# Kernel tuning notes

Measured on AMD Instinct MI355X. Metric: run time of the kernel, lower is better.

## Reference

```python
import jax, jax.numpy as jnp
import numpy as np

B, S, CIN = 16384, 24, 10
NH, DK, DM = 16, 8, 256
DV = DM // NH  # 16
EPS = 1e-5
T_POS = 1000.0


def _ln(x, g, b):
    mu = jnp.mean(x, axis=-1, keepdims=True)
    var = jnp.mean((x - mu) ** 2, axis=-1, keepdims=True)
    return (x - mu) * jax.lax.rsqrt(var + EPS) * g + b


def _bn(x, g, b, m, v):
    # eval-mode BatchNorm1d over channel (last) dim
    return (x - m) * jax.lax.rsqrt(v + EPS) * g + b


def setup_inputs() -> dict:
    key = jax.random.key(0)
    ks = jax.random.split(key, 16)
    x = jax.random.normal(ks[0], (B, S, CIN + 1), dtype=jnp.float32)
    pos = jax.random.uniform(ks[1], (B, S), dtype=jnp.float32) * 365.0
    x = x.at[:, :, 0].set(pos)
    w = lambda k, shp, s=0.05: (jax.random.normal(k, shp, dtype=jnp.float32) * s)
    d = {
        'x': x,
        'ln1_g': jnp.ones((CIN,), jnp.float32), 'ln1_b': jnp.zeros((CIN,), jnp.float32),
        'conv_w': w(ks[2], (DM, CIN)), 'conv_b': jnp.zeros((DM,), jnp.float32),
        'bn1_g': jnp.ones((DM,), jnp.float32), 'bn1_b': jnp.zeros((DM,), jnp.float32),
        'bn1_m': jnp.zeros((DM,), jnp.float32), 'bn1_v': jnp.ones((DM,), jnp.float32),
        'Q': w(ks[3], (NH, DK), float(np.sqrt(2.0 / DK))),
        'Wk': w(ks[4], (NH * DK, DM), float(np.sqrt(2.0 / DK))), 'bk': jnp.zeros((NH * DK,), jnp.float32),
        'W1': w(ks[5], (128, 256)), 'b1': jnp.zeros((128,), jnp.float32),
        'bn2_g': jnp.ones((128,), jnp.float32), 'bn2_b': jnp.zeros((128,), jnp.float32),
        'bn2_m': jnp.zeros((128,), jnp.float32), 'bn2_v': jnp.ones((128,), jnp.float32),
        'oln_g': jnp.ones((128,), jnp.float32), 'oln_b': jnp.zeros((128,), jnp.float32),
        'Wd1': w(ks[6], (64, 128)), 'bd1': jnp.zeros((64,), jnp.float32),
        'bnd1_g': jnp.ones((64,), jnp.float32), 'bnd1_b': jnp.zeros((64,), jnp.float32),
        'bnd1_m': jnp.zeros((64,), jnp.float32), 'bnd1_v': jnp.ones((64,), jnp.float32),
        'Wd2': w(ks[7], (32, 64)), 'bd2': jnp.zeros((32,), jnp.float32),
        'bnd2_g': jnp.ones((32,), jnp.float32), 'bnd2_b': jnp.zeros((32,), jnp.float32),
        'bnd2_m': jnp.zeros((32,), jnp.float32), 'bnd2_v': jnp.ones((32,), jnp.float32),
        'Wd3': w(ks[8], (20, 32)), 'bd3': jnp.zeros((20,), jnp.float32),
    }
    return d


def reference(x, ln1_g, ln1_b, conv_w, conv_b, bn1_g, bn1_b, bn1_m, bn1_v,
              Q, Wk, bk, W1, b1, bn2_g, bn2_b, bn2_m, bn2_v, oln_g, oln_b,
              Wd1, bd1, bnd1_g, bnd1_b, bnd1_m, bnd1_v,
              Wd2, bd2, bnd2_g, bnd2_b, bnd2_m, bnd2_v, Wd3, bd3):
    pos = x[:, :, 0]            # (B, S) positions
    feat = x[:, :, 1:]          # (B, S, CIN)
    feat = _ln(feat, ln1_g, ln1_b)
    # inconv: 1x1 Conv1d == per-timestep Linear, then eval BatchNorm1d over channels
    h = jnp.einsum('bsc,dc->bsd', feat, conv_w) + conv_b
    h = _bn(h, bn1_g, bn1_b, bn1_m, bn1_v)
    # sinusoid positional encoding, interleaved sin/cos
    div = jnp.exp(jnp.arange(0, DM, 2, dtype=jnp.float32) * (-np.log(T_POS) / DM))  # (DM/2,)
    ang = pos[:, :, None] * div                                   # (B, S, DM/2)
    pe = jnp.stack([jnp.sin(ang), jnp.cos(ang)], axis=-1).reshape(pos.shape[0], pos.shape[1], DM)
    e = h + pe                                                    # (B, S, DM)
    # LTAE multi-head attention with shared learned query
    k = jnp.einsum('bsd,hkd->bshk', e, Wk.reshape(NH, DK, DM)) + bk.reshape(NH, DK)
    logits = jnp.einsum('hk,bshk->bhs', Q, k) / np.sqrt(DK)
    attn = jax.nn.softmax(logits, axis=-1)                        # (B, NH, S); dropout=eval
    v = e.reshape(e.shape[0], e.shape[1], NH, DV)                 # head-chunked values
    o = jnp.einsum('bhs,bshc->bhc', attn, v).reshape(e.shape[0], NH * DV)  # (B, 256)
    # MLP3: Linear(256,128) + BN + ReLU, then dropout(eval) + LayerNorm
    m = jax.nn.relu(_bn(o @ W1.T + b1, bn2_g, bn2_b, bn2_m, bn2_v))
    m = _ln(m, oln_g, oln_b)
    # decoder: [128,64,32,20]
    d1 = jax.nn.relu(_bn(m @ Wd1.T + bd1, bnd1_g, bnd1_b, bnd1_m, bnd1_v))
    d2 = jax.nn.relu(_bn(d1 @ Wd2.T + bd2, bnd2_g, bnd2_b, bnd2_m, bnd2_v))
    out = d2 @ Wd3.T + bd3                                        # (B, 20)
    return out
```

## Files before the change

### kernel.cpp

```cpp
#include <hip/hip_runtime.h>
#include <hip/hip_bf16.h>


typedef __attribute__((ext_vector_type(8))) short bf16x8;
typedef __attribute__((ext_vector_type(4))) float f32x4;

#define EPS 1e-5f
#define INV_SQRT8 0.35355339059327373f
#define KDIV (-0.07785768972392256f)
#define INV2PI 0.15915494309189535f
#define LOG2E 1.4426950408889634f

__device__ __forceinline__ unsigned short f2bf(float f){
  union { float f; unsigned u; } v; v.f = f;
  unsigned r = v.u + 0x7FFFu + ((v.u >> 16) & 1u);
  return (unsigned short)(r >> 16);
}
__device__ __forceinline__ float bf2f(unsigned short h){
  union { unsigned u; float f; } v; v.u = ((unsigned)h) << 16; return v.f;
}
__device__ __forceinline__ float asf(unsigned u){
  union { unsigned u; float f; } v; v.u = u; return v.f;
}
__device__ __forceinline__ unsigned pk2bf(float lo, float hi){
  __hip_bfloat162 h2 = __float22bfloat162_rn(make_float2(lo, hi));
  return *reinterpret_cast<unsigned*>(&h2);
}

__global__ __launch_bounds__(256) void k0_pre(
    const float* __restrict__ conv_w, const float* __restrict__ conv_b,
    const float* __restrict__ bn1_g, const float* __restrict__ bn1_b,
    const float* __restrict__ bn1_m, const float* __restrict__ bn1_v,
    const float* __restrict__ Q, const float* __restrict__ Wk,
    const float* __restrict__ bk,
    const float* __restrict__ W1, const float* __restrict__ b1,
    const float* __restrict__ bn2_g, const float* __restrict__ bn2_b,
    const float* __restrict__ bn2_m, const float* __restrict__ bn2_v,
    const float* __restrict__ oln_g, const float* __restrict__ oln_b,
    const float* __restrict__ Wd1, const float* __restrict__ bd1,
    const float* __restrict__ bnd1_g, const float* __restrict__ bnd1_b,
    const float* __restrict__ bnd1_m, const float* __restrict__ bnd1_v,
    const float* __restrict__ Wd2, const float* __restrict__ bd2,
    const float* __restrict__ bnd2_g, const float* __restrict__ bnd2_b,
    const float* __restrict__ bnd2_m, const float* __restrict__ bnd2_v,
    const float* __restrict__ Wd3,
    unsigned short* __restrict__ wqF, unsigned short* __restrict__ w1F,
    unsigned short* __restrict__ wd1F, unsigned short* __restrict__ wd2F,
    unsigned short* __restrict__ wd3F,
    float* __restrict__ convwT, float* __restrict__ convbE,
    float* __restrict__ biasq, float* __restrict__ b1E,
    float* __restrict__ bd1E, float* __restrict__ bd2E)
{
  __shared__ float redL[256];
  const int t = threadIdx.x;
  const int bid = blockIdx.x;

  if (bid < 64){
    for (int e = bid*512 + t; e < bid*512 + 512; e += 256){
      int j = e & 7, lj = (e >> 3) & 63, kc = (e >> 9) & 7, nt = (e >> 12) & 7;
      int n = nt*16 + (lj & 15);
      int k = kc*32 + ((lj >> 4) << 3) + j;
      float s2 = bn2_g[n] * rsqrtf(bn2_v[n] + EPS);
      w1F[e] = f2bf(W1[n*256 + k] * s2);
    }
  } else if (bid < 68){
    int base = (bid - 64)*2048;
    #pragma unroll 4
    for (int it = 0; it < 8; ++it){
      int e = base + it*256 + t;
      int j = e & 7, lj = (e >> 3) & 63, kc = (e >> 9) & 3, nt = (e >> 11) & 3;
      int n = nt*16 + (lj & 15);
      int k = kc*32 + ((lj >> 4) << 3) + j;
      float sd = bnd1_g[n] * rsqrtf(bnd1_v[n] + EPS);
      wd1F[e] = f2bf(Wd1[n*128 + k] * sd * oln_g[k]);
    }
  } else if (bid == 68){
    #pragma unroll 4
    for (int it = 0; it < 8; ++it){
      int e = it*256 + t;
      int j = e & 7, lj = (e >> 3) & 63, kc = (e >> 9) & 1, nt = (e >> 10) & 1;
      int n = nt*16 + (lj & 15);
      int k = kc*32 + ((lj >> 4) << 3) + j;
      float sd = bnd2_g[n] * rsqrtf(bnd2_v[n] + EPS);
      wd2F[e] = f2bf(Wd2[n*64 + k] * sd);
    }
  } else if (bid == 69){
    #pragma unroll
    for (int it = 0; it < 4; ++it){
      int e = it*256 + t;
      int j = e & 7, lj = (e >> 3) & 63, nt = (e >> 9) & 1;
      int n = nt*16 + (lj & 15);
      int k = ((lj >> 4) << 3) + j;
      float v = (n < 20) ? Wd3[n*32 + k] : 0.f;
      wd3F[e] = f2bf(v);
    }
  } else if (bid == 70){
    #pragma unroll 4
    for (int it = 0; it < 16; ++it){
      int e = it*256 + t;
      int j = e & 7, lj = (e >> 3) & 63, kc = (e >> 9) & 7;
      int h = lj & 15;
      int dd = kc*32 + ((lj >> 4) << 3) + j;
      float acc = 0.f;
      #pragma unroll
      for (int kk = 0; kk < 8; ++kk)
        acc += Q[h*8+kk] * Wk[(h*8+kk)*256 + dd];
      wqF[e] = f2bf(acc * INV_SQRT8);
    }
  } else if (bid == 71){
    __shared__ float wqL[16*257];
    __shared__ float coefL[256*12];
    __shared__ float QL[128];
    __shared__ float bkL[128];
    wqF[4096 + t] = 0; wqF[4096 + 256 + t] = 0;
    if (t < 128){ QL[t] = Q[t]; bkL[t] = bk[t]; }
    __syncthreads();
    {
      const int d = t;
      float s1 = bn1_g[d] * rsqrtf(bn1_v[d] + EPS);
      #pragma unroll
      for (int c = 0; c < 10; ++c) coefL[d*12 + c] = conv_w[d*10 + c] * s1;
      coefL[d*12 + 10] = conv_b[d]*s1 + bn1_b[d] - bn1_m[d]*s1;
      coefL[d*12 + 11] = 0.f;
      #pragma unroll 4
      for (int h = 0; h < 16; ++h){
        float acc = 0.f;
        #pragma unroll
        for (int kk = 0; kk < 8; ++kk)
          acc += QL[h*8+kk] * Wk[(h*8+kk)*256 + d];
        wqL[h*257 + d] = acc;
      }
    }
    __syncthreads();
    if (t < 176){
      int h = t / 11, cc = t - h*11;
      const float* wq = wqL + h*257;
      float acc = 0.f;
      #pragma unroll 4
      for (int d2 = 0; d2 < 256; ++d2)
        acc += coefL[d2*12 + cc] * wq[d2];
      acc *= INV_SQRT8;
      if (cc < 10){
        int lane = (cc < 8) ? h : (16 + h);
        int j = cc & 7;
        wqF[4096 + lane*8 + j] = f2bf(acc);
      } else {
        float qb = 0.f;
        #pragma unroll
        for (int kk = 0; kk < 8; ++kk) qb += QL[h*8+kk]*bkL[h*8+kk];
        biasq[h] = acc + qb * INV_SQRT8;
      }
    }
  } else if (bid == 72){
    #pragma unroll
    for (int it = 0; it < 10; ++it){
      int e = it*256 + t;
      int c = e >> 8, d = e & 255;
      float s1 = bn1_g[d] * rsqrtf(bn1_v[d] + EPS);
      convwT[e] = conv_w[d*10 + c] * s1;
    }
  } else if (bid == 73){
    {
      int d = t;
      float s1 = bn1_g[d] * rsqrtf(bn1_v[d] + EPS);
      convbE[d] = conv_b[d]*s1 + bn1_b[d] - bn1_m[d]*s1;
    }
    if (t < 128){
      float s2 = bn2_g[t] * rsqrtf(bn2_v[t] + EPS);
      b1E[t] = b1[t]*s2 + bn2_b[t] - bn2_m[t]*s2;
    }
    if (t < 32){
      float sd = bnd2_g[t] * rsqrtf(bnd2_v[t] + EPS);
      bd2E[t] = bd2[t]*sd + bnd2_b[t] - bnd2_m[t]*sd;
    }
  } else {
    int n = t >> 2, si = t & 3;
    float acc = 0.f;
    #pragma unroll 8
    for (int i2 = 0; i2 < 32; ++i2){
      int i = si*32 + i2;
      acc += oln_b[i] * Wd1[n*128 + i];
    }
    redL[t] = acc;
    __syncthreads();
    if (t < 64){
      float sd = bnd1_g[t] * rsqrtf(bnd1_v[t] + EPS);
      float a = redL[4*t] + redL[4*t+1] + redL[4*t+2] + redL[4*t+3];
      bd1E[t] = bd1[t]*sd + bnd1_b[t] - bnd1_m[t]*sd + a*sd;
    }
  }
}

__global__ __launch_bounds__(256, 4) void k1_attn(
    const float* __restrict__ x, const float* __restrict__ ln1_g,
    const float* __restrict__ ln1_b,
    const unsigned short* __restrict__ wqF, const float* __restrict__ convwT,
    const float* __restrict__ convbE, const float* __restrict__ biasq,
    unsigned short* __restrict__ o_frag)
{
  __shared__ unsigned short peR[48*264];
  __shared__ float attnF[2*16*25];
  __shared__ unsigned short featn[48*16];
  __shared__ float xL[528];
  __shared__ float divL[128];
  __shared__ __align__(16) unsigned short zeroB[8];
  float* gL = xL;

  const int t = threadIdx.x;
  const int b0 = blockIdx.x * 2;
  const int w = t >> 6, l = t & 63;

  if (t < 132)
    *(float4*)(xL + t*4) = *(const float4*)(x + (size_t)b0*264 + t*4);
  if (t < 128) divL[t] = exp2f((float)t * KDIV) * INV2PI;
  if (t < 8) zeroB[t] = 0;
  __syncthreads();

  if (w == 3){
    if (l < 48){
      const float* xr = xL + l*11;
      float f[10]; float mu = 0.f;
      #pragma unroll
      for (int c = 0; c < 10; ++c){ f[c] = xr[1+c]; mu += f[c]; }
      mu *= 0.1f;
      float var = 0.f;
      #pragma unroll
      for (int c = 0; c < 10; ++c){ float dv = f[c]-mu; var += dv*dv; }
      var *= 0.1f;
      float rs = rsqrtf(var + EPS);
      float fn[10];
      #pragma unroll
      for (int c = 0; c < 10; ++c) fn[c] = (f[c]-mu)*rs*ln1_g[c] + ln1_b[c];
      #pragma unroll
      for (int q = 0; q < 5; ++q)
        *(unsigned*)(featn + l*16 + 2*q) = pk2bf(fn[2*q], fn[2*q+1]);
      #pragma unroll
      for (int z = 0; z < 3; ++z)
        *(unsigned*)(featn + l*16 + 10 + 2*z) = 0u;
    }
  }

  f32x4 acc = {0.f,0.f,0.f,0.f};
  const int m = l & 15, g = l >> 4;
  if (w < 3){
    const int mt = w;
    const int row = mt*16 + m;
    const float p = xL[row*11];
    #pragma unroll
    for (int kc = 0; kc < 8; ++kc){
      float4 dv4 = *(const float4*)(divL + kc*16 + g*4);
      unsigned pk[4];
      #pragma unroll
      for (int q = 0; q < 4; ++q){
        float dv = (q==0)?dv4.x:(q==1)?dv4.y:(q==2)?dv4.z:dv4.w;
        float ang = p * dv;
        float fr = ang - floorf(ang);
        float sv = __builtin_amdgcn_sinf(fr);
        float cv = __builtin_amdgcn_cosf(fr);
        pk[q] = pk2bf(sv, cv);
      }
      union { bf16x8 v; uint4 u; } af;
      af.u = make_uint4(pk[0], pk[1], pk[2], pk[3]);
      *(uint4*)(peR + row*264 + (kc*4+g)*8) = af.u;
      bf16x8 b = *(const bf16x8*)(wqF + ((size_t)(kc*64 + l))*8);
      acc = __builtin_amdgcn_mfma_f32_16x16x32_bf16(af.v, b, acc, 0, 0, 0);
    }
  }
  __syncthreads();

  if (w < 3){
    const int mt = w;
    {
      const unsigned short* ap = (g < 2) ? (featn + (mt*16 + m)*16 + g*8)
                                         : zeroB;
      bf16x8 a = *(const bf16x8*)ap;
      bf16x8 b = *(const bf16x8*)(wqF + ((size_t)(8*64 + l))*8);
      acc = __builtin_amdgcn_mfma_f32_16x16x32_bf16(a, b, acc, 0, 0, 0);
    }
    const int h = m;
    float bq = biasq[h];
    #pragma unroll
    for (int reg = 0; reg < 4; ++reg){
      int row = mt*16 + g*4 + reg;
      int bb = row >= 24; int s = row - bb*24;
      attnF[(bb*16+h)*25 + s] = acc[reg] + bq;
    }
  }
  __syncthreads();

  {
    const int bh = t >> 3, ln = t & 7;
    float* L = attnF + bh*25;
    float v0 = L[ln], v1 = L[ln+8], v2 = L[ln+16];
    float mx = fmaxf(fmaxf(v0, v1), v2);
    mx = fmaxf(mx, __shfl_xor(mx, 1, 64));
    mx = fmaxf(mx, __shfl_xor(mx, 2, 64));
    mx = fmaxf(mx, __shfl_xor(mx, 4, 64));
    float p0 = exp2f((v0-mx)*LOG2E);
    float p1 = exp2f((v1-mx)*LOG2E);
    float p2 = exp2f((v2-mx)*LOG2E);
    float sm = p0 + p1 + p2;
    sm += __shfl_xor(sm, 1, 64);
    sm += __shfl_xor(sm, 2, 64);
    sm += __shfl_xor(sm, 4, 64);
    float inv = 1.f / sm;
    L[ln] = p0*inv; L[ln+8] = p1*inv; L[ln+16] = p2*inv;
  }
  __syncthreads();

  if (t < 160){
    int bb = t / 80; int rem = t - bb*80;
    int h = rem / 5, c = rem - h*5;
    const float* A = attnF + (bb*16+h)*25;
    float g0 = 0.f, g1 = 0.f;
    for (int s = 0; s < 24; ++s){
      float a = A[s];
      const unsigned short* fr = featn + (bb*24+s)*16;
      g0 += a * bf2f(fr[c]);
      g1 += a * bf2f(fr[c+5]);
    }
    gL[(bb*16+h)*12 + c]     = g0;
    gL[(bb*16+h)*12 + c + 5] = g1;
  }
  __syncthreads();

  {
    const int bb = t >> 7, dp = t & 127;
    const int d0 = dp*2, h = dp >> 3;
    float2 o2 = *(const float2*)(convbE + d0);
    const float* gp = gL + (bb*16+h)*12;
    #pragma unroll
    for (int c = 0; c < 10; ++c){
      float2 cw = *(const float2*)(convwT + c*256 + d0);
      o2.x += cw.x * gp[c];
      o2.y += cw.y * gp[c];
    }
    const float* A = attnF + (bb*16+h)*25;
    const unsigned short* pr = peR + bb*24*264 + d0;
    #pragma unroll
    for (int s = 0; s < 24; ++s){
      unsigned u = *(const unsigned*)(pr + s*264);
      float a = A[s];
      o2.x += a * asf(u << 16);
      o2.y += a * asf(u & 0xFFFF0000u);
    }
    const int row = b0 + bb;
    const int rt = row >> 4, mm = row & 15;
    const int kc = d0 >> 5, gg = (d0 >> 3) & 3, j = d0 & 7;
    *(unsigned*)(o_frag + ((size_t)((rt*8+kc)*64 + gg*16 + mm))*8 + j)
        = pk2bf(o2.x, o2.y);
  }
}

__global__ __launch_bounds__(256, 4) void k2_mlp(
    const unsigned short* __restrict__ o_frag,
    const unsigned short* __restrict__ w1F, const float* __restrict__ b1E,
    const unsigned short* __restrict__ wd1F, const float* __restrict__ bd1E,
    const unsigned short* __restrict__ wd2F, const float* __restrict__ bd2E,
    const unsigned short* __restrict__ wd3F, const float* __restrict__ bd3,
    float* __restrict__ out)
{
  __shared__ float mL[16*132];
  __shared__ unsigned short mh[16*136];
  __shared__ unsigned short d1L[16*72];
  __shared__ unsigned short d2L[16*40];
  __shared__ float redL[64];
  __shared__ float stats[32];

  const int t = threadIdx.x;
  const int w = t >> 6, l = t & 63;
  const size_t rowBase = (size_t)blockIdx.x * 16;
  const int rt = blockIdx.x;
  const int g8  = (l >> 4) << 3;
  const int c15 = l & 15;

  {
    f32x4 acc[2];
    { f32x4 z = {0.f,0.f,0.f,0.f}; acc[0] = z; acc[1] = z; }
    #pragma unroll
    for (int kc = 0; kc < 8; ++kc){
      bf16x8 a = *(const bf16x8*)(o_frag + ((size_t)((rt*8+kc)*64 + l))*8);
      #pragma unroll
      for (int n2 = 0; n2 < 2; ++n2){
        int nt = 2*w + n2;
        bf16x8 b = *(const bf16x8*)(w1F + ((size_t)((nt*8+kc)*64 + l))*8);
        acc[n2] = __builtin_amdgcn_mfma_f32_16x16x32_bf16(a, b, acc[n2], 0,0,0);
      }
    }
    #pragma unroll
    for (int n2 = 0; n2 < 2; ++n2){
      int col = (2*w + n2)*16 + c15;
      float be = b1E[col];
      #pragma unroll
      for (int reg = 0; reg < 4; ++reg){
        int row = ((l>>4)<<2) + reg;
        mL[row*132 + col] = fmaxf(acc[n2][reg] + be, 0.f);
      }
    }
  }
  __syncthreads();

  if (t < 32){
    const float* R = mL + (t>>1)*132 + (t&1)*64;
    float s = 0.f, q = 0.f;
    for (int k = 0; k < 64; ++k){ float v = R[k]; s += v; q += v*v; }
    redL[t*2] = s; redL[t*2+1] = q;
  }
  __syncthreads();
  if (t < 16){
    float s = redL[4*t] + redL[4*t+2];
    float q = redL[4*t+1] + redL[4*t+3];
    float mu = s * (1.f/128.f);
    float var = q * (1.f/128.f) - mu*mu;
    stats[2*t] = mu; stats[2*t+1] = rsqrtf(var + EPS);
  }
  __syncthreads();

  {
    int r = t >> 4, run = t & 15;
    float mu = stats[2*r], rs = stats[2*r+1];
    const float* R = mL + r*132 + run*8;
    unsigned pk[4];
    #pragma unroll
    for (int q = 0; q < 4; ++q)
      pk[q] = pk2bf((R[2*q]-mu)*rs, (R[2*q+1]-mu)*rs);
    *(uint4*)(mh + r*136 + run*8) = make_uint4(pk[0], pk[1], pk[2], pk[3]);
  }
  __syncthreads();

  {
    const int nt = w;
    f32x4 acc = {0.f,0.f,0.f,0.f};
    #pragma unroll
    for (int kc = 0; kc < 4; ++kc){
      bf16x8 b = *(const bf16x8*)(wd1F + ((size_t)((nt*4+kc)*64 + l))*8);
      bf16x8 a = *(const bf16x8*)(mh + c15*136 + kc*32 + g8);
      acc = __builtin_amdgcn_mfma_f32_16x16x32_bf16(a, b, acc, 0,0,0);
    }
    int col = nt*16 + c15;
    float be = bd1E[col];
    #pragma unroll
    for (int reg = 0; reg < 4; ++reg){
      int row = ((l>>4)<<2) + reg;
      d1L[row*72 + col] = f2bf(fmaxf(acc[reg] + be, 0.f));
    }
  }
  __syncthreads();

  if (w < 2){
    const int nt = w;
    f32x4 acc = {0.f,0.f,0.f,0.f};
    #pragma unroll
    for (int kc = 0; kc < 2; ++kc){
      bf16x8 a = *(const bf16x8*)(d1L + c15*72 + kc*32 + g8);
      bf16x8 b = *(const bf16x8*)(wd2F + ((size_t)((nt*2+kc)*64 + l))*8);
      acc = __builtin_amdgcn_mfma_f32_16x16x32_bf16(a, b, acc, 0,0,0);
    }
    int col = nt*16 + c15;
    float be = bd2E[col];
    #pragma unroll
    for (int reg = 0; reg < 4; ++reg){
      int row = ((l>>4)<<2) + reg;
      d2L[row*40 + col] = f2bf(fmaxf(acc[reg] + be, 0.f));
    }
  }
  __syncthreads();

  if (w < 2){
    const int nt = w;
    bf16x8 a = *(const bf16x8*)(d2L + c15*40 + g8);
    bf16x8 b = *(const bf16x8*)(wd3F + ((size_t)(nt*64 + l))*8);
    f32x4 acc = {0.f,0.f,0.f,0.f};
    acc = __builtin_amdgcn_mfma_f32_16x16x32_bf16(a, b, acc, 0,0,0);
    int col = nt*16 + c15;
    if (col < 20){
      float be = bd3[col];
      #pragma unroll
      for (int reg = 0; reg < 4; ++reg){
        int row = ((l>>4)<<2) + reg;
        out[(rowBase + row)*20 + col] = acc[reg] + be;
      }
    }
  }
}

extern "C" void kernel_launch(void* const* d_in, const int* in_sizes, int n_in,
                              void* d_out, int out_size, void* d_ws, size_t ws_size,
                              hipStream_t stream)
{
  (void)in_sizes; (void)n_in; (void)out_size; (void)ws_size;
  const float* x      = (const float*)d_in[0];
  const float* ln1_g  = (const float*)d_in[1];
  const float* ln1_b  = (const float*)d_in[2];
  const float* conv_w = (const float*)d_in[3];
  const float* conv_b = (const float*)d_in[4];
  const float* bn1_g  = (const float*)d_in[5];
  const float* bn1_b  = (const float*)d_in[6];
  const float* bn1_m  = (const float*)d_in[7];
  const float* bn1_v  = (const float*)d_in[8];
  const float* Q      = (const float*)d_in[9];
  const float* Wk     = (const float*)d_in[10];
  const float* bk     = (const float*)d_in[11];
  const float* W1     = (const float*)d_in[12];
  const float* b1     = (const float*)d_in[13];
  const float* bn2_g  = (const float*)d_in[14];
  const float* bn2_b  = (const float*)d_in[15];
  const float* bn2_m  = (const float*)d_in[16];
  const float* bn2_v  = (const float*)d_in[17];
  const float* oln_g  = (const float*)d_in[18];
  const float* oln_b  = (const float*)d_in[19];
  const float* Wd1    = (const float*)d_in[20];
  const float* bd1    = (const float*)d_in[21];
  const float* bnd1_g = (const float*)d_in[22];
  const float* bnd1_b = (const float*)d_in[23];
  const float* bnd1_m = (const float*)d_in[24];
  const float* bnd1_v = (const float*)d_in[25];
  const float* Wd2    = (const float*)d_in[26];
  const float* bd2    = (const float*)d_in[27];
  const float* bnd2_g = (const float*)d_in[28];
  const float* bnd2_b = (const float*)d_in[29];
  const float* bnd2_m = (const float*)d_in[30];
  const float* bnd2_v = (const float*)d_in[31];
  const float* Wd3    = (const float*)d_in[32];
  const float* bd3    = (const float*)d_in[33];

  char* ws = (char*)d_ws;
  unsigned short* wqF  = (unsigned short*)(ws + 0);
  unsigned short* w1F  = (unsigned short*)(ws + 9216);
  unsigned short* wd1F = (unsigned short*)(ws + 74752);
  unsigned short* wd2F = (unsigned short*)(ws + 91136);
  unsigned short* wd3F = (unsigned short*)(ws + 95232);
  float* convwT = (float*)(ws + 97280);
  float* convbE = (float*)(ws + 107520);
  float* biasq  = (float*)(ws + 108544);
  float* b1E    = (float*)(ws + 108608);
  float* bd1E   = (float*)(ws + 109120);
  float* bd2E   = (float*)(ws + 109376);
  unsigned short* o_frag = (unsigned short*)(ws + 109568);

  hipLaunchKernelGGL(k0_pre, dim3(75), dim3(256), 0, stream,
      conv_w, conv_b, bn1_g, bn1_b, bn1_m, bn1_v, Q, Wk, bk,
      W1, b1, bn2_g, bn2_b, bn2_m, bn2_v, oln_g, oln_b,
      Wd1, bd1, bnd1_g, bnd1_b, bnd1_m, bnd1_v,
      Wd2, bd2, bnd2_g, bnd2_b, bnd2_m, bnd2_v, Wd3,
      wqF, w1F, wd1F, wd2F, wd3F, convwT, convbE, biasq, b1E, bd1E, bd2E);

  hipLaunchKernelGGL(k1_attn, dim3(8192), dim3(256), 0, stream,
      x, ln1_g, ln1_b, wqF, convwT, convbE, biasq, o_frag);

  hipLaunchKernelGGL(k2_mlp, dim3(1024), dim3(256), 0, stream,
      o_frag, w1F, b1E, wd1F, bd1E, wd2F, bd2E, wd3F, bd3, (float*)d_out);
}
```

Baseline: 186.0 us.

## Spread positional-encoding generation over all warps and use MFMA for attention-weighted features

Positional-encoding sin/cos generation now runs across all four warps instead of three, and the attention-logit MFMA reads the encoding back from shared memory after a barrier. The attention-weighted feature reduction is recast as a 16x16x32 bf16 MFMA per batch element, replacing a scalar loop over 160 threads. Attention rows are also packed at stride 24 so they can be read with float4 loads into registers. The intent is better warp balance and fewer scalar LDS reads, at the cost of an extra shared-memory round trip and bf16 rounding of the attention weights in the feature path.

```diff
diff --git a/kernel.cpp b/kernel.cpp
--- a/kernel.cpp
+++ b/kernel.cpp
@@ -198,12 +198,11 @@
     const float* __restrict__ convbE, const float* __restrict__ biasq,
     unsigned short* __restrict__ o_frag)
 {
-  __shared__ unsigned short peR[48*264];
-  __shared__ float attnF[2*16*25];
-  __shared__ unsigned short featn[48*16];
-  __shared__ float xL[528];
-  __shared__ float divL[128];
-  __shared__ __align__(16) unsigned short zeroB[8];
+  __shared__ __align__(16) unsigned short peR[48*264];
+  __shared__ __align__(16) float attnF[32*24];
+  __shared__ __align__(16) unsigned short featn[48*16];
+  __shared__ __align__(16) float divL[128];
+  __shared__ __align__(16) float xL[536];
   float* gL = xL;
 
   const int t = threadIdx.x;
@@ -212,85 +211,82 @@
 
   if (t < 132)
     *(float4*)(xL + t*4) = *(const float4*)(x + (size_t)b0*264 + t*4);
+  else if (t < 134)
+    *(float4*)(xL + 528 + (t-132)*4) = make_float4(0.f,0.f,0.f,0.f);
   if (t < 128) divL[t] = exp2f((float)t * KDIV) * INV2PI;
-  if (t < 8) zeroB[t] = 0;
-  __syncthreads();
-
-  if (w == 3){
-    if (l < 48){
-      const float* xr = xL + l*11;
-      float f[10]; float mu = 0.f;
-      #pragma unroll
-      for (int c = 0; c < 10; ++c){ f[c] = xr[1+c]; mu += f[c]; }
-      mu *= 0.1f;
-      float var = 0.f;
-      #pragma unroll
-      for (int c = 0; c < 10; ++c){ float dv = f[c]-mu; var += dv*dv; }
-      var *= 0.1f;
-      float rs = rsqrtf(var + EPS);
-      float fn[10];
-      #pragma unroll
-      for (int c = 0; c < 10; ++c) fn[c] = (f[c]-mu)*rs*ln1_g[c] + ln1_b[c];
-      #pragma unroll
-      for (int q = 0; q < 5; ++q)
-        *(unsigned*)(featn + l*16 + 2*q) = pk2bf(fn[2*q], fn[2*q+1]);
-      #pragma unroll
-      for (int z = 0; z < 3; ++z)
-        *(unsigned*)(featn + l*16 + 10 + 2*z) = 0u;
-    }
-  }
-
-  f32x4 acc = {0.f,0.f,0.f,0.f};
+  __syncthreads();
+
+  {
+    const int g = (l >> 4) & 3, rlo = l & 15;
+    #pragma unroll
+    for (int it = 0; it < 6; ++it){
+      int combo = it*4 + w;
+      int mt = combo >> 3, kc = combo & 7;
+      int row = mt*16 + rlo;
+      int run = kc*4 + g;
+      float p = xL[row*11];
+      unsigned pk[4];
+      #pragma unroll
+      for (int q = 0; q < 4; ++q){
+        float fr = __builtin_amdgcn_fractf(p * divL[run*4 + q]);
+        pk[q] = pk2bf(__builtin_amdgcn_sinf(fr), __builtin_amdgcn_cosf(fr));
+      }
+      *(uint4*)(peR + row*264 + run*8) = make_uint4(pk[0], pk[1], pk[2], pk[3]);
+    }
+  }
+  if (w == 3 && l < 48){
+    const float* xr = xL + l*11;
+    float f[10]; float mu = 0.f;
+    #pragma unroll
+    for (int c = 0; c < 10; ++c){ f[c] = xr[1+c]; mu += f[c]; }
+    mu *= 0.1f;
+    float var = 0.f;
+    #pragma unroll
+    for (int c = 0; c < 10; ++c){ float dv = f[c]-mu; var += dv*dv; }
+    var *= 0.1f;
+    float rs = rsqrtf(var + EPS);
+    float fn[10];
+    #pragma unroll
+    for (int c = 0; c < 10; ++c) fn[c] = (f[c]-mu)*rs*ln1_g[c] + ln1_b[c];
+    #pragma unroll
+    for (int q = 0; q < 5; ++q)
+      *(unsigned*)(featn + l*16 + 2*q) = pk2bf(fn[2*q], fn[2*q+1]);
+    #pragma unroll
+    for (int z = 0; z < 3; ++z)
+      *(unsigned*)(featn + l*16 + 10 + 2*z) = 0u;
+  }
+  __syncthreads();
+
   const int m = l & 15, g = l >> 4;
   if (w < 3){
     const int mt = w;
-    const int row = mt*16 + m;
-    const float p = xL[row*11];
+    f32x4 acc = {0.f,0.f,0.f,0.f};
     #pragma unroll
     for (int kc = 0; kc < 8; ++kc){
-      float4 dv4 = *(const float4*)(divL + kc*16 + g*4);
-      unsigned pk[4];
-      #pragma unroll
-      for (int q = 0; q < 4; ++q){
-        float dv = (q==0)?dv4.x:(q==1)?dv4.y:(q==2)?dv4.z:dv4.w;
-        float ang = p * dv;
-        float fr = ang - floorf(ang);
-        float sv = __builtin_amdgcn_sinf(fr);
-        float cv = __builtin_amdgcn_cosf(fr);
-        pk[q] = pk2bf(sv, cv);
-      }
-      union { bf16x8 v; uint4 u; } af;
-      af.u = make_uint4(pk[0], pk[1], pk[2], pk[3]);
-      *(uint4*)(peR + row*264 + (kc*4+g)*8) = af.u;
+      bf16x8 a = *(const bf16x8*)(peR + (mt*16 + m)*264 + kc*32 + g*8);
       bf16x8 b = *(const bf16x8*)(wqF + ((size_t)(kc*64 + l))*8);
-      acc = __builtin_amdgcn_mfma_f32_16x16x32_bf16(af.v, b, acc, 0, 0, 0);
-    }
-  }
-  __syncthreads();
-
-  if (w < 3){
-    const int mt = w;
+      acc = __builtin_amdgcn_mfma_f32_16x16x32_bf16(a, b, acc, 0, 0, 0);
+    }
     {
       const unsigned short* ap = (g < 2) ? (featn + (mt*16 + m)*16 + g*8)
-                                         : zeroB;
+                                         : (const unsigned short*)(xL + 528);
       bf16x8 a = *(const bf16x8*)ap;
       bf16x8 b = *(const bf16x8*)(wqF + ((size_t)(8*64 + l))*8);
       acc = __builtin_amdgcn_mfma_f32_16x16x32_bf16(a, b, acc, 0, 0, 0);
     }
-    const int h = m;
-    float bq = biasq[h];
+    float bq = biasq[m];
     #pragma unroll
     for (int reg = 0; reg < 4; ++reg){
       int row = mt*16 + g*4 + reg;
       int bb = row >= 24; int s = row - bb*24;
-      attnF[(bb*16+h)*25 + s] = acc[reg] + bq;
+      attnF[(bb*16+m)*24 + s] = acc[reg] + bq;
     }
   }
   __syncthreads();
 
   {
     const int bh = t >> 3, ln = t & 7;
-    float* L = attnF + bh*25;
+    float* L = attnF + bh*24;
     float v0 = L[ln], v1 = L[ln+8], v2 = L[ln+16];
     float mx = fmaxf(fmaxf(v0, v1), v2);
     mx = fmaxf(mx, __shfl_xor(mx, 1, 64));
@@ -308,19 +304,34 @@
   }
   __syncthreads();
 
-  if (t < 160){
-    int bb = t / 80; int rem = t - bb*80;
-    int h = rem / 5, c = rem - h*5;
-    const float* A = attnF + (bb*16+h)*25;
-    float g0 = 0.f, g1 = 0.f;
-    for (int s = 0; s < 24; ++s){
-      float a = A[s];
-      const unsigned short* fr = featn + (bb*24+s)*16;
-      g0 += a * bf2f(fr[c]);
-      g1 += a * bf2f(fr[c+5]);
-    }
-    gL[(bb*16+h)*12 + c]     = g0;
-    gL[(bb*16+h)*12 + c + 5] = g1;
+  if (w < 2){
+    const int bb = w;
+    const int q = g;
+    union { bf16x8 v; unsigned u[4]; } aF;
+    if (q < 3){
+      const float* ap = attnF + (bb*16 + m)*24 + q*8;
+      float4 a0 = *(const float4*)ap;
+      float4 a1 = *(const float4*)(ap + 4);
+      aF.u[0] = pk2bf(a0.x, a0.y); aF.u[1] = pk2bf(a0.z, a0.w);
+      aF.u[2] = pk2bf(a1.x, a1.y); aF.u[3] = pk2bf(a1.z, a1.w);
+    } else {
+      aF.u[0] = 0u; aF.u[1] = 0u; aF.u[2] = 0u; aF.u[3] = 0u;
+    }
+    union { bf16x8 v; unsigned short s[8]; } bF;
+    #pragma unroll
+    for (int j = 0; j < 8; ++j){
+      int s = q*8 + j;
+      bF.s[j] = (s < 24) ? featn[(bb*24 + s)*16 + m] : (unsigned short)0;
+    }
+    f32x4 z = {0.f,0.f,0.f,0.f};
+    f32x4 ga = __builtin_amdgcn_mfma_f32_16x16x32_bf16(aF.v, bF.v, z, 0,0,0);
+    if (m < 12){
+      #pragma unroll
+      for (int reg = 0; reg < 4; ++reg){
+        int h = q*4 + reg;
+        gL[(bb*16+h)*12 + m] = ga[reg];
+      }
+    }
   }
   __syncthreads();
 
@@ -335,14 +346,19 @@
       o2.x += cw.x * gp[c];
       o2.y += cw.y * gp[c];
     }
-    const float* A = attnF + (bb*16+h)*25;
+    float A[24];
+    {
+      const float* Ab = attnF + (bb*16+h)*24;
+      #pragma unroll
+      for (int q4 = 0; q4 < 6; ++q4)
+        *(float4*)(A + q4*4) = *(const float4*)(Ab + q4*4);
+    }
     const unsigned short* pr = peR + bb*24*264 + d0;
     #pragma unroll
     for (int s = 0; s < 24; ++s){
       unsigned u = *(const unsigned*)(pr + s*264);
-      float a = A[s];
-      o2.x += a * asf(u << 16);
-      o2.y += a * asf(u & 0xFFFF0000u);
+      o2.x += A[s] * asf(u << 16);
+      o2.y += A[s] * asf(u & 0xFFFF0000u);
     }
     const int row = b0 + bb;
     const int rt = row >> 4, mm = row & 15;
```

After: 183.9 us. Within noise of the previous version (-1.1%).
